# Performance work log

Hardware: AMD Instinct MI355X
Metric: run time of the kernel (lower is better)

The kernel has to match this reference:

```python
import jax, jax.numpy as jnp
import numpy as np

EPS = 1e-5

def layer_norm(x, g, b):
    mu = jnp.mean(x, axis=-1, keepdims=True)
    var = jnp.var(x, axis=-1, keepdims=True)
    return (x - mu) * jax.lax.rsqrt(var + EPS) * g + b

def setup_inputs() -> dict:
    key = jax.random.key(0)
    ks = jax.random.split(key, 12)
    B, N, D, H = 32, 577, 768, 12
    Dh = D // H
    hid = 4 * D
    s = lambda d: 1.0 / np.sqrt(d)
    return {
        "x": jax.random.normal(ks[0], (B, N, D), jnp.float32),
        "ln1_g": jnp.ones((D,), jnp.float32),
        "ln1_b": jnp.zeros((D,), jnp.float32),
        "ln2_g": jnp.ones((D,), jnp.float32),
        "ln2_b": jnp.zeros((D,), jnp.float32),
        "w_qkv": jax.random.normal(ks[1], (D, 3 * D), jnp.float32) * s(D),
        "b_qkv": jnp.zeros((3 * D,), jnp.float32),
        "w_proj": jax.random.normal(ks[2], (D, D), jnp.float32) * s(D),
        "b_proj": jnp.zeros((D,), jnp.float32),
        "w_fc1": jax.random.normal(ks[3], (D, hid), jnp.float32) * s(D),
        "b_fc1": jnp.zeros((hid,), jnp.float32),
        "w_fc2": jax.random.normal(ks[4], (hid, D), jnp.float32) * s(hid),
        "b_fc2": jnp.zeros((D,), jnp.float32),
    }

def reference(x, ln1_g, ln1_b, ln2_g, ln2_b, w_qkv, b_qkv, w_proj, b_proj,
              w_fc1, b_fc1, w_fc2, b_fc2):
    B, N, D = x.shape
    H = 12
    Dh = D // H
    scale = Dh ** -0.5
    # --- attention branch ---
    h = layer_norm(x, ln1_g, ln1_b)
    qkv = h @ w_qkv + b_qkv                      # [B, N, 3D]
    qkv = qkv.reshape(B, N, 3, H, Dh).transpose(2, 0, 3, 1, 4)  # [3, B, H, N, Dh]
    q, k, v = qkv[0], qkv[1], qkv[2]
    attn = jnp.einsum('bhnd,bhmd->bhnm', q, k) * scale  # [B, H, N, N]
    attn = jax.nn.softmax(attn, axis=-1)
    o = jnp.einsum('bhnm,bhmd->bhnd', attn, v)           # [B, H, N, Dh]
    o = o.transpose(0, 2, 1, 3).reshape(B, N, D)
    o = o @ w_proj + b_proj
    x = x + o
    # --- MLP branch ---
    h = layer_norm(x, ln2_g, ln2_b)
    h = jnp.clip(h @ w_fc1 + b_fc1, 0.0, 6.0)            # ReLU6
    h = h @ w_fc2 + b_fc2
    return x + h
```

## Files before the change

### kernel.cpp

```cpp
#include <hip/hip_runtime.h>
#include <math.h>


typedef unsigned short u16;
typedef _Float16 f16;
typedef __attribute__((ext_vector_type(8))) _Float16 f16x8;
typedef __attribute__((ext_vector_type(4))) float f32x4;

__device__ __forceinline__ u16 f2h(float x) {
    union { f16 h; u16 u; } cv;
    cv.h = (f16)x;
    return cv.u;
}
__device__ __forceinline__ float h2f(u16 b) {
    union { u16 u; f16 h; } cv;
    cv.u = b;
    return (float)cv.h;
}
__device__ __forceinline__ void load_lds16(const u16* g, void* l) {
    __builtin_amdgcn_global_load_lds(
        (const __attribute__((address_space(1))) void*)g,
        (__attribute__((address_space(3))) void*)l, 16, 0, 0);
}
__device__ __forceinline__ int xcd_swz(int lid, int nwg) {
    const int x = lid & 7, pos = lid >> 3;
    const int q = nwg >> 3, r = nwg & 7;
    return (x < r ? x * (q + 1) : r * (q + 1) + (x - r) * q) + pos;
}

__global__ __launch_bounds__(256)
void wprep_kernel(const float* __restrict__ W, u16* __restrict__ Th,
                  int K, int N)
{
    __shared__ float t[32][33];
    const int n0 = blockIdx.x * 32, k0 = blockIdx.y * 32;
    const int tr = threadIdx.x >> 3, tc4 = (threadIdx.x & 7) * 4;
    const float4 v = *(const float4*)&W[(size_t)(k0 + tr) * N + n0 + tc4];
    t[tr][tc4 + 0] = v.x; t[tr][tc4 + 1] = v.y;
    t[tr][tc4 + 2] = v.z; t[tr][tc4 + 3] = v.w;
    __syncthreads();
    ushort4 h;
    h.x = f2h(t[tc4 + 0][tr]);
    h.y = f2h(t[tc4 + 1][tr]);
    h.z = f2h(t[tc4 + 2][tr]);
    h.w = f2h(t[tc4 + 3][tr]);
    *(ushort4*)&Th[(size_t)(n0 + tr) * K + k0 + tc4] = h;
}

__global__ __launch_bounds__(256)
void ln_kernel(const float* __restrict__ x, const float* __restrict__ g,
               const float* __restrict__ beta, u16* __restrict__ oh, int pad)
{
    const int row = blockIdx.x;
    const int tid = threadIdx.x;
    const float* xr = x + (size_t)row * 768;
    const float v0 = xr[tid], v1 = xr[tid + 256], v2 = xr[tid + 512];
    float s  = v0 + v1 + v2;
    float ss = v0 * v0 + v1 * v1 + v2 * v2;
    #pragma unroll
    for (int off = 1; off < 64; off <<= 1) {
        s  += __shfl_xor(s, off);
        ss += __shfl_xor(ss, off);
    }
    __shared__ float redS[4], redQ[4];
    const int wid = tid >> 6;
    if ((tid & 63) == 0) { redS[wid] = s; redQ[wid] = ss; }
    __syncthreads();
    s  = redS[0] + redS[1] + redS[2] + redS[3];
    ss = redQ[0] + redQ[1] + redQ[2] + redQ[3];
    const float mean = s * (1.0f / 768.0f);
    const float var  = ss * (1.0f / 768.0f) - mean * mean;
    const float rstd = rsqrtf(var + 1e-5f);
    int row_p = row;
    if (pad) {
        const unsigned bb = (unsigned)row / 577u;
        row_p = (int)(bb * 640u + ((unsigned)row - bb * 577u));
    }
    u16* ohr = oh + (size_t)row_p * 768;
    #pragma unroll
    for (int u = 0; u < 3; ++u) {
        const int c = tid + u * 256;
        const float vv = (u == 0) ? v0 : (u == 1) ? v1 : v2;
        ohr[c] = f2h((vv - mean) * rstd * g[c] + beta[c]);
    }
}

template<int RELU6, int RES, int OMODE, int PADMAP>
__global__ __launch_bounds__(256)
void mfma_gemm(const u16* __restrict__ Ah, const u16* __restrict__ Bh,
               const float* __restrict__ bias, const float* res,
               float* Cf, u16* __restrict__ Ch,
               u16* __restrict__ Qh_, u16* __restrict__ Kh_,
               u16* __restrict__ Vth_,
               int M, int N, int K)
{
    __shared__ u16 lds[32768];

    const int tid  = threadIdx.x;
    const int wave = tid >> 6;
    const int lane = tid & 63;

    const int nwg = gridDim.x * gridDim.y;
    int lid = blockIdx.y * gridDim.x + blockIdx.x;
    lid = xcd_swz(lid, nwg);
    const int bm = (lid / gridDim.x) * 128;
    const int bn = (lid % gridDim.x) * 128;

    const int rl = lane >> 2;
    const int c  = lane & 3;
    const int r0 = wave * 16 + rl;
    const int r1 = 64 + r0;
    const int kgA0 = (((r0 >> 3) & 1) << 2) | (c ^ ((r0 >> 1) & 3));
    const int kgA1 = (((r1 >> 3) & 1) << 2) | (c ^ ((r1 >> 1) & 3));

    const u16* pA00 = Ah + (size_t)(bm + r0) * K + kgA0 * 8;
    const u16* pA01 = Ah + (size_t)(bm + r0) * K + (kgA0 ^ 4) * 8;
    const u16* pA10 = Ah + (size_t)(bm + r1) * K + kgA1 * 8;
    const u16* pA11 = Ah + (size_t)(bm + r1) * K + (kgA1 ^ 4) * 8;
    const u16* pB00 = Bh + (size_t)(bn + r0) * K + kgA0 * 8;
    const u16* pB01 = Bh + (size_t)(bn + r0) * K + (kgA0 ^ 4) * 8;
    const u16* pB10 = Bh + (size_t)(bn + r1) * K + kgA1 * 8;
    const u16* pB11 = Bh + (size_t)(bn + r1) * K + (kgA1 ^ 4) * 8;

    char* ldsb = (char*)lds;
    char* dA00 = ldsb +     0 + wave * 1024;
    char* dA01 = ldsb +  8192 + wave * 1024;
    char* dA10 = ldsb +  4096 + wave * 1024;
    char* dA11 = ldsb + 12288 + wave * 1024;
    char* dB00 = ldsb + 16384 + wave * 1024;
    char* dB01 = ldsb + 24576 + wave * 1024;
    char* dB10 = ldsb + 20480 + wave * 1024;
    char* dB11 = ldsb + 28672 + wave * 1024;

    const int am0 = (wave >> 1) * 64;
    const int bn0 = (wave & 1) * 64;
    const int l15 = lane & 15;
    const int lg  = lane >> 4;

    f32x4 acc[4][4] = {};
    const int np = K >> 6;

    load_lds16(pA00, dA00); load_lds16(pA01, dA01);
    load_lds16(pA10, dA10); load_lds16(pA11, dA11);
    load_lds16(pB00, dB00); load_lds16(pB01, dB01);
    load_lds16(pB10, dB10); load_lds16(pB11, dB11);
    pA00 += 64; pA01 += 64; pA10 += 64; pA11 += 64;
    pB00 += 64; pB01 += 64; pB10 += 64; pB11 += 64;

    int cur = 0;
    for (int p = 0; p < np; ++p) {
        asm volatile("s_waitcnt vmcnt(0)" ::: "memory");
        __builtin_amdgcn_s_barrier();
        if (p + 1 < np) {
            const int o = (cur ^ 1) << 15;
            load_lds16(pA00, dA00 + o); load_lds16(pA01, dA01 + o);
            load_lds16(pA10, dA10 + o); load_lds16(pA11, dA11 + o);
            load_lds16(pB00, dB00 + o); load_lds16(pB01, dB01 + o);
            load_lds16(pB10, dB10 + o); load_lds16(pB11, dB11 + o);
            pA00 += 64; pA01 += 64; pA10 += 64; pA11 += 64;
            pB00 += 64; pB01 += 64; pB10 += 64; pB11 += 64;
        }
        const u16* sA = lds + (cur << 14);
        const u16* sB = sA + 8192;

        #pragma unroll
        for (int ss = 0; ss < 2; ++ss) {
            f16x8 ah[4];
            #pragma unroll
            for (int fm = 0; fm < 4; ++fm) {
                const int ar = am0 + fm * 16 + l15;
                const int kg = ss * 4 + lg;
                const int pc = (kg & 3) ^ ((ar >> 1) & 3);
                const int pt = (kg >> 2) ^ ((ar >> 3) & 1);
                ah[fm] = *(const f16x8*)&sA[pt * 4096 + ar * 32 + pc * 8];
            }
            #pragma unroll
            for (int fn = 0; fn < 4; ++fn) {
                const int br = bn0 + fn * 16 + l15;
                const int kg = ss * 4 + lg;
                const int pc = (kg & 3) ^ ((br >> 1) & 3);
                const int pt = (kg >> 2) ^ ((br >> 3) & 1);
                const f16x8 bh = *(const f16x8*)&sB[pt * 4096 + br * 32 + pc * 8];
                #pragma unroll
                for (int fm = 0; fm < 4; ++fm)
                    acc[fm][fn] = __builtin_amdgcn_mfma_f32_16x16x32_f16(
                        ah[fm], bh, acc[fm][fn], 0, 0, 0);
            }
        }
        cur ^= 1;
    }

    if (OMODE == 2) {
        __syncthreads();
        const int s  = bn / 768;
        const int hh = ((bn + bn0) - s * 768) >> 6;
        const int gr0 = bm + am0;
        const int bb  = gr0 / 640;
        const int n0  = gr0 - bb * 640;
        u16* eph = lds + wave * 4352;
        #pragma unroll
        for (int fn = 0; fn < 4; ++fn) {
            const float bv = bias[bn + bn0 + fn * 16 + l15];
            #pragma unroll
            for (int fm = 0; fm < 4; ++fm) {
                const f32x4 v = acc[fm][fn];
                #pragma unroll
                for (int j = 0; j < 4; ++j) {
                    const float o = v[j] + bv;
                    const int idx = (s == 2)
                        ? (fn * 16 + l15) * 68 + fm * 16 + lg * 4 + j
                        : (fm * 16 + lg * 4 + j) * 68 + fn * 16 + l15;
                    eph[idx] = f2h(o);
                }
            }
        }
        __syncthreads();
        if (s == 2) {
            u16* dh = Vth_ + (size_t)(bb * 12 + hh) * 64 * 640 + n0 + lane;
            #pragma unroll 8
            for (int d = 0; d < 64; ++d)
                dh[(size_t)d * 640] = eph[d * 68 + lane];
        } else {
            u16* base = ((s == 0) ? Qh_ : Kh_) +
                        ((size_t)(bb * 12 + hh) * 640 + n0) * 64 + lane;
            #pragma unroll 8
            for (int rr = 0; rr < 64; ++rr)
                base[(size_t)rr * 64] = eph[rr * 68 + lane];
        }
    } else {
        #pragma unroll
        for (int fn = 0; fn < 4; ++fn) {
            const int cc = bn + bn0 + fn * 16 + l15;
            const float bv = bias[cc];
            #pragma unroll
            for (int fm = 0; fm < 4; ++fm) {
                const int rbase = bm + am0 + fm * 16 + lg * 4;
                const f32x4 v = acc[fm][fn];
                #pragma unroll
                for (int j = 0; j < 4; ++j) {
                    const int r = rbase + j;
                    if (PADMAP) {
                        const int bb = r / 640;
                        const int nn = r - bb * 640;
                        if (nn < 577) {
                            const size_t ro = (size_t)(bb * 577 + nn) * N + cc;
                            float o = v[j] + bv;
                            if (RELU6) o = fminf(fmaxf(o, 0.0f), 6.0f);
                            if (RES)   o += res[ro];
                            Cf[ro] = o;
                        }
                    } else if (r < M) {
                        float o = v[j] + bv;
                        if (RELU6) o = fminf(fmaxf(o, 0.0f), 6.0f);
                        if (RES)   o += res[(size_t)r * N + cc];
                        if (OMODE == 0) Cf[(size_t)r * N + cc] = o;
                        else            Ch[(size_t)r * N + cc] = f2h(o);
                    }
                }
            }
        }
    }
}

__global__ __launch_bounds__(256)
void attn_mfma(const u16* __restrict__ Qh, const u16* __restrict__ Kh,
               const u16* __restrict__ Vth, u16* __restrict__ Oh)
{
    constexpr int SEQ = 577, NP = 640;
    __shared__ u16 sK[2 * 4096], sV[2 * 4096];
    __shared__ u16 sPh[4][16 * 72];

    const int tid  = threadIdx.x;
    const int wave = tid >> 6;
    const int lane = tid & 63;
    const int l15 = lane & 15, lg = lane >> 4;

    const int nwg = gridDim.x * gridDim.y;
    int lid = blockIdx.y * gridDim.x + blockIdx.x;
    lid = xcd_swz(lid, nwg);
    const int q0 = (lid % gridDim.x) * 64;
    const int bh = lid / gridDim.x;

    const size_t qkBase = (size_t)bh * NP * 64;
    const size_t vBase  = (size_t)bh * 64 * NP;

    f16x8 qfh[2];
    {
        const size_t ro = qkBase + (size_t)(q0 + wave * 16 + l15) * 64;
        #pragma unroll
        for (int ks = 0; ks < 2; ++ks)
            qfh[ks] = *(const f16x8*)&Qh[ro + (ks * 4 + lg) * 8];
    }

    const int srow = lane >> 3;
    const int sc   = lane & 7;

    f32x4 oacc[4] = {};
    float mrun = -1e30f, lrun = 0.0f;
    constexpr int NT = 10;

    #pragma unroll
    for (int t = 0; t < 2; ++t) {
        const int row = wave * 16 + t * 8 + srow;
        const int lc  = sc ^ (row & 7);
        load_lds16(Kh + qkBase + (size_t)row * 64 + lc * 8,
                   (char*)sK + wave * 2048 + t * 1024);
        load_lds16(Vth + vBase + (size_t)row * NP + lc * 8,
                   (char*)sV + wave * 2048 + t * 1024);
    }
    __syncthreads();

    int cur = 0;
    for (int it = 0; it < NT; ++it) {
        const int kv0 = it * 64;
        if (it + 1 < NT) {
            const int nkv = kv0 + 64;
            const int o = (cur ^ 1) * 8192;
            #pragma unroll
            for (int t = 0; t < 2; ++t) {
                const int row = wave * 16 + t * 8 + srow;
                const int lc  = sc ^ (row & 7);
                load_lds16(Kh + qkBase + (size_t)(nkv + row) * 64 + lc * 8,
                           (char*)sK + o + wave * 2048 + t * 1024);
                load_lds16(Vth + vBase + (size_t)row * NP + nkv + lc * 8,
                           (char*)sV + o + wave * 2048 + t * 1024);
            }
        }
        const u16* sKc = sK + cur * 4096;
        const u16* sVc = sV + cur * 4096;

        f32x4 sacc[4] = {};
        __builtin_amdgcn_s_setprio(1);
        #pragma unroll
        for (int fkv = 0; fkv < 4; ++fkv) {
            const int row = fkv * 16 + l15;
            #pragma unroll
            for (int ks = 0; ks < 2; ++ks) {
                const int ph = ((ks * 4 + lg) ^ (row & 7)) * 8;
                const f16x8 kh = *(const f16x8*)&sKc[row * 64 + ph];
                sacc[fkv] = __builtin_amdgcn_mfma_f32_16x16x32_f16(
                    kh, qfh[ks], sacc[fkv], 0, 0, 0);
            }
        }
        __builtin_amdgcn_s_setprio(0);

        float p[4][4];
        float mt = -1e30f;
        const bool tail = (kv0 + 64 > SEQ);
        #pragma unroll
        for (int fkv = 0; fkv < 4; ++fkv)
            #pragma unroll
            for (int j = 0; j < 4; ++j) {
                float sv = sacc[fkv][j] * 0.125f;
                if (tail && (kv0 + fkv * 16 + lg * 4 + j >= SEQ)) sv = -1e30f;
                p[fkv][j] = sv;
                mt = fmaxf(mt, sv);
            }
        mt = fmaxf(mt, __shfl_xor(mt, 16));
        mt = fmaxf(mt, __shfl_xor(mt, 32));
        const float mnew = fmaxf(mrun, mt);
        const float corr = __expf(mrun - mnew);
        float rs = 0.0f;
        #pragma unroll
        for (int fkv = 0; fkv < 4; ++fkv)
            #pragma unroll
            for (int j = 0; j < 4; ++j) {
                p[fkv][j] = __expf(p[fkv][j] - mnew);
                rs += p[fkv][j];
            }
        rs += __shfl_xor(rs, 16);
        rs += __shfl_xor(rs, 32);
        lrun = lrun * corr + rs;
        mrun = mnew;
        #pragma unroll
        for (int fd = 0; fd < 4; ++fd)
            #pragma unroll
            for (int j = 0; j < 4; ++j) oacc[fd][j] *= corr;

        u16* phr = &sPh[wave][l15 * 72];
        #pragma unroll
        for (int fkv = 0; fkv < 4; ++fkv) {
            ushort4 hv;
            hv.x = f2h(p[fkv][0]);
            hv.y = f2h(p[fkv][1]);
            hv.z = f2h(p[fkv][2]);
            hv.w = f2h(p[fkv][3]);
            *(ushort4*)&phr[fkv * 16 + lg * 4] = hv;
        }

        __builtin_amdgcn_s_setprio(1);
        #pragma unroll
        for (int ks = 0; ks < 2; ++ks) {
            const f16x8 pbh = *(const f16x8*)&sPh[wave][l15 * 72 + (ks * 4 + lg) * 8];
            #pragma unroll
            for (int fd = 0; fd < 4; ++fd) {
                const int row = fd * 16 + l15;
                const int ph = ((ks * 4 + lg) ^ (row & 7)) * 8;
                const f16x8 vh = *(const f16x8*)&sVc[row * 64 + ph];
                oacc[fd] = __builtin_amdgcn_mfma_f32_16x16x32_f16(
                    vh, pbh, oacc[fd], 0, 0, 0);
            }
        }
        __builtin_amdgcn_s_setprio(0);

        __syncthreads();
        cur ^= 1;
    }

    const int q = q0 + wave * 16 + l15;
    if (q < SEQ) {
        const float inv = 1.0f / lrun;
        const int b = bh / 12, h = bh % 12;
        const size_t rowo = ((size_t)(b * 640 + q)) * 768 + h * 64;
        #pragma unroll
        for (int fd = 0; fd < 4; ++fd) {
            ushort4 hv;
            hv.x = f2h(oacc[fd][0] * inv);
            hv.y = f2h(oacc[fd][1] * inv);
            hv.z = f2h(oacc[fd][2] * inv);
            hv.w = f2h(oacc[fd][3] * inv);
            *(ushort4*)&Oh[rowo + fd * 16 + lg * 4] = hv;
        }
    }
}

extern "C" void kernel_launch(void* const* d_in, const int* in_sizes, int n_in,
                              void* d_out, int out_size, void* d_ws, size_t ws_size,
                              hipStream_t stream)
{
    const float* x      = (const float*)d_in[0];
    const float* ln1_g  = (const float*)d_in[1];
    const float* ln1_b  = (const float*)d_in[2];
    const float* ln2_g  = (const float*)d_in[3];
    const float* ln2_b  = (const float*)d_in[4];
    const float* w_qkv  = (const float*)d_in[5];
    const float* b_qkv  = (const float*)d_in[6];
    const float* w_proj = (const float*)d_in[7];
    const float* b_proj = (const float*)d_in[8];
    const float* w_fc1  = (const float*)d_in[9];
    const float* b_fc1  = (const float*)d_in[10];
    const float* w_fc2  = (const float*)d_in[11];
    const float* b_fc2  = (const float*)d_in[12];
    float* out = (float*)d_out;

    const int M  = 18464;
    const int Mq = 20480;

    char* p = (char*)d_ws;
    u16* Wqkv  = (u16*)p;    p += (size_t)2304 * 768 * 2;
    u16* Wproj = (u16*)p;    p += (size_t)768 * 768 * 2;
    u16* Wfc1  = (u16*)p;    p += (size_t)3072 * 768 * 2;
    u16* Wfc2  = (u16*)p;    p += (size_t)768 * 3072 * 2;
    u16* A_h = (u16*)p;      p += (size_t)Mq * 768 * 2;
    u16* Qh  = (u16*)p;      p += (size_t)384 * 640 * 64 * 2;
    u16* Kh  = (u16*)p;      p += (size_t)384 * 640 * 64 * 2;
    u16* Vth = (u16*)p;      p += (size_t)384 * 64 * 640 * 2;
    u16* fc1h = Qh;

    wprep_kernel<<<dim3(72, 24),  256, 0, stream>>>(w_qkv,  Wqkv,  768, 2304);
    wprep_kernel<<<dim3(24, 24),  256, 0, stream>>>(w_proj, Wproj, 768, 768);
    wprep_kernel<<<dim3(96, 24),  256, 0, stream>>>(w_fc1,  Wfc1,  768, 3072);
    wprep_kernel<<<dim3(24, 96),  256, 0, stream>>>(w_fc2,  Wfc2,  3072, 768);

    ln_kernel<<<M, 256, 0, stream>>>(x, ln1_g, ln1_b, A_h, 1);
    mfma_gemm<0, 0, 2, 0><<<dim3(18, 160), 256, 0, stream>>>(
        A_h, Wqkv, b_qkv, nullptr, nullptr, nullptr,
        Qh, Kh, Vth, Mq, 2304, 768);
    attn_mfma<<<dim3(10, 384), 256, 0, stream>>>(Qh, Kh, Vth, A_h);
    mfma_gemm<0, 1, 0, 1><<<dim3(6, 160), 256, 0, stream>>>(
        A_h, Wproj, b_proj, x, out, nullptr,
        nullptr, nullptr, nullptr, Mq, 768, 768);
    ln_kernel<<<M, 256, 0, stream>>>(out, ln2_g, ln2_b, A_h, 0);
    const int CH = 9344;
    for (int r0 = 0; r0 < M; r0 += CH) {
        const int mc = (M - r0 < CH) ? (M - r0) : CH;
        const int mtiles = (mc + 127) / 128;
        mfma_gemm<1, 0, 1, 0><<<dim3(24, mtiles), 256, 0, stream>>>(
            A_h + (size_t)r0 * 768, Wfc1, b_fc1, nullptr, nullptr, fc1h,
            nullptr, nullptr, nullptr, mc, 3072, 768);
        mfma_gemm<0, 1, 0, 0><<<dim3(6, mtiles), 256, 0, stream>>>(
            fc1h, Wfc2, b_fc2, out + (size_t)r0 * 768, out + (size_t)r0 * 768,
            nullptr, nullptr, nullptr, nullptr, mc, 768, 3072);
    }
}
```

Before: 624.2 us.

## Use 4-stage K=32 LDS pipeline in GEMM and drop MLP row chunking

Measured after the change: 649.5 us. +4.1%, slower.

```diff
diff --git a/kernel.cpp b/kernel.cpp
--- a/kernel.cpp
+++ b/kernel.cpp
@@ -106,31 +106,22 @@
     const int bm = (lid / gridDim.x) * 128;
     const int bn = (lid % gridDim.x) * 128;
 
-    const int rl = lane >> 2;
+    const int r0 = wave * 16 + (lane >> 2);
+    const int r1 = 64 + r0;
     const int c  = lane & 3;
-    const int r0 = wave * 16 + rl;
-    const int r1 = 64 + r0;
-    const int kgA0 = (((r0 >> 3) & 1) << 2) | (c ^ ((r0 >> 1) & 3));
-    const int kgA1 = (((r1 >> 3) & 1) << 2) | (c ^ ((r1 >> 1) & 3));
-
-    const u16* pA00 = Ah + (size_t)(bm + r0) * K + kgA0 * 8;
-    const u16* pA01 = Ah + (size_t)(bm + r0) * K + (kgA0 ^ 4) * 8;
-    const u16* pA10 = Ah + (size_t)(bm + r1) * K + kgA1 * 8;
-    const u16* pA11 = Ah + (size_t)(bm + r1) * K + (kgA1 ^ 4) * 8;
-    const u16* pB00 = Bh + (size_t)(bn + r0) * K + kgA0 * 8;
-    const u16* pB01 = Bh + (size_t)(bn + r0) * K + (kgA0 ^ 4) * 8;
-    const u16* pB10 = Bh + (size_t)(bn + r1) * K + kgA1 * 8;
-    const u16* pB11 = Bh + (size_t)(bn + r1) * K + (kgA1 ^ 4) * 8;
+    const int kg0 = c ^ ((r0 >> 1) & 3);
+    const int kg1 = c ^ ((r1 >> 1) & 3);
+
+    const u16* pA0 = Ah + (size_t)(bm + r0) * K + 8 * kg0;
+    const u16* pA1 = Ah + (size_t)(bm + r1) * K + 8 * kg1;
+    const u16* pB0 = Bh + (size_t)(bn + r0) * K + 8 * kg0;
+    const u16* pB1 = Bh + (size_t)(bn + r1) * K + 8 * kg1;
 
     char* ldsb = (char*)lds;
-    char* dA00 = ldsb +     0 + wave * 1024;
-    char* dA01 = ldsb +  8192 + wave * 1024;
-    char* dA10 = ldsb +  4096 + wave * 1024;
-    char* dA11 = ldsb + 12288 + wave * 1024;
-    char* dB00 = ldsb + 16384 + wave * 1024;
-    char* dB01 = ldsb + 24576 + wave * 1024;
-    char* dB10 = ldsb + 20480 + wave * 1024;
-    char* dB11 = ldsb + 28672 + wave * 1024;
+    char* dA0 = ldsb +     0 + wave * 1024;
+    char* dA1 = ldsb +  4096 + wave * 1024;
+    char* dB0 = ldsb +  8192 + wave * 1024;
+    char* dB1 = ldsb + 12288 + wave * 1024;
 
     const int am0 = (wave >> 1) * 64;
     const int bn0 = (wave & 1) * 64;
@@ -138,56 +129,47 @@
     const int lg  = lane >> 4;
 
     f32x4 acc[4][4] = {};
-    const int np = K >> 6;
-
-    load_lds16(pA00, dA00); load_lds16(pA01, dA01);
-    load_lds16(pA10, dA10); load_lds16(pA11, dA11);
-    load_lds16(pB00, dB00); load_lds16(pB01, dB01);
-    load_lds16(pB10, dB10); load_lds16(pB11, dB11);
-    pA00 += 64; pA01 += 64; pA10 += 64; pA11 += 64;
-    pB00 += 64; pB01 += 64; pB10 += 64; pB11 += 64;
-
-    int cur = 0;
-    for (int p = 0; p < np; ++p) {
-        asm volatile("s_waitcnt vmcnt(0)" ::: "memory");
+    const int nk = K >> 5;
+
+    #pragma unroll
+    for (int s = 0; s < 3; ++s) {
+        const int o = s << 14;
+        load_lds16(pA0, dA0 + o); load_lds16(pA1, dA1 + o);
+        load_lds16(pB0, dB0 + o); load_lds16(pB1, dB1 + o);
+        pA0 += 32; pA1 += 32; pB0 += 32; pB1 += 32;
+    }
+
+    for (int ks = 0; ks < nk; ++ks) {
+        if (ks + 2 < nk)      asm volatile("s_waitcnt vmcnt(8)" ::: "memory");
+        else if (ks + 1 < nk) asm volatile("s_waitcnt vmcnt(4)" ::: "memory");
+        else                  asm volatile("s_waitcnt vmcnt(0)" ::: "memory");
         __builtin_amdgcn_s_barrier();
-        if (p + 1 < np) {
-            const int o = (cur ^ 1) << 15;
-            load_lds16(pA00, dA00 + o); load_lds16(pA01, dA01 + o);
-            load_lds16(pA10, dA10 + o); load_lds16(pA11, dA11 + o);
-            load_lds16(pB00, dB00 + o); load_lds16(pB01, dB01 + o);
-            load_lds16(pB10, dB10 + o); load_lds16(pB11, dB11 + o);
-            pA00 += 64; pA01 += 64; pA10 += 64; pA11 += 64;
-            pB00 += 64; pB01 += 64; pB10 += 64; pB11 += 64;
-        }
-        const u16* sA = lds + (cur << 14);
-        const u16* sB = sA + 8192;
-
-        #pragma unroll
-        for (int ss = 0; ss < 2; ++ss) {
-            f16x8 ah[4];
-            #pragma unroll
-            for (int fm = 0; fm < 4; ++fm) {
-                const int ar = am0 + fm * 16 + l15;
-                const int kg = ss * 4 + lg;
-                const int pc = (kg & 3) ^ ((ar >> 1) & 3);
-                const int pt = (kg >> 2) ^ ((ar >> 3) & 1);
-                ah[fm] = *(const f16x8*)&sA[pt * 4096 + ar * 32 + pc * 8];
-            }
-            #pragma unroll
-            for (int fn = 0; fn < 4; ++fn) {
-                const int br = bn0 + fn * 16 + l15;
-                const int kg = ss * 4 + lg;
-                const int pc = (kg & 3) ^ ((br >> 1) & 3);
-                const int pt = (kg >> 2) ^ ((br >> 3) & 1);
-                const f16x8 bh = *(const f16x8*)&sB[pt * 4096 + br * 32 + pc * 8];
-                #pragma unroll
-                for (int fm = 0; fm < 4; ++fm)
-                    acc[fm][fn] = __builtin_amdgcn_mfma_f32_16x16x32_f16(
-                        ah[fm], bh, acc[fm][fn], 0, 0, 0);
-            }
-        }
-        cur ^= 1;
+        if (ks + 3 < nk) {
+            const int o = ((ks + 3) & 3) << 14;
+            load_lds16(pA0, dA0 + o); load_lds16(pA1, dA1 + o);
+            load_lds16(pB0, dB0 + o); load_lds16(pB1, dB1 + o);
+            pA0 += 32; pA1 += 32; pB0 += 32; pB1 += 32;
+        }
+        const u16* sA = lds + ((ks & 3) << 13);
+        const u16* sB = sA + 4096;
+
+        f16x8 ah[4];
+        #pragma unroll
+        for (int fm = 0; fm < 4; ++fm) {
+            const int ar = am0 + fm * 16 + l15;
+            const int ph = (lg ^ ((ar >> 1) & 3)) * 8;
+            ah[fm] = *(const f16x8*)&sA[ar * 32 + ph];
+        }
+        #pragma unroll
+        for (int fn = 0; fn < 4; ++fn) {
+            const int br = bn0 + fn * 16 + l15;
+            const int ph = (lg ^ ((br >> 1) & 3)) * 8;
+            const f16x8 bh = *(const f16x8*)&sB[br * 32 + ph];
+            #pragma unroll
+            for (int fm = 0; fm < 4; ++fm)
+                acc[fm][fn] = __builtin_amdgcn_mfma_f32_16x16x32_f16(
+                    ah[fm], bh, acc[fm][fn], 0, 0, 0);
+        }
     }
 
     if (OMODE == 2) {
@@ -455,7 +437,7 @@
     u16* Qh  = (u16*)p;      p += (size_t)384 * 640 * 64 * 2;
     u16* Kh  = (u16*)p;      p += (size_t)384 * 640 * 64 * 2;
     u16* Vth = (u16*)p;      p += (size_t)384 * 64 * 640 * 2;
-    u16* fc1h = Qh;
+    u16* fc1h = (u16*)p;     p += (size_t)18560 * 3072 * 2;
 
     wprep_kernel<<<dim3(72, 24),  256, 0, stream>>>(w_qkv,  Wqkv,  768, 2304);
     wprep_kernel<<<dim3(24, 24),  256, 0, stream>>>(w_proj, Wproj, 768, 768);
@@ -471,15 +453,10 @@
         A_h, Wproj, b_proj, x, out, nullptr,
         nullptr, nullptr, nullptr, Mq, 768, 768);
     ln_kernel<<<M, 256, 0, stream>>>(out, ln2_g, ln2_b, A_h, 0);
-    const int CH = 9344;
-    for (int r0 = 0; r0 < M; r0 += CH) {
-        const int mc = (M - r0 < CH) ? (M - r0) : CH;
-        const int mtiles = (mc + 127) / 128;
-        mfma_gemm<1, 0, 1, 0><<<dim3(24, mtiles), 256, 0, stream>>>(
-            A_h + (size_t)r0 * 768, Wfc1, b_fc1, nullptr, nullptr, fc1h,
-            nullptr, nullptr, nullptr, mc, 3072, 768);
-        mfma_gemm<0, 1, 0, 0><<<dim3(6, mtiles), 256, 0, stream>>>(
-            fc1h, Wfc2, b_fc2, out + (size_t)r0 * 768, out + (size_t)r0 * 768,
-            nullptr, nullptr, nullptr, nullptr, mc, 768, 3072);
-    }
-}
+    mfma_gemm<1, 0, 1, 0><<<dim3(24, 145), 256, 0, stream>>>(
+        A_h, Wfc1, b_fc1, nullptr, nullptr, fc1h,
+        nullptr, nullptr, nullptr, M, 3072, 768);
+    mfma_gemm<0, 1, 0, 0><<<dim3(6, 145), 256, 0, stream>>>(
+        fc1h, Wfc2, b_fc2, out, out, nullptr,
+        nullptr, nullptr, nullptr, M, 768, 3072);
+}
```
